# Kernel optimization log

Measured on AMD Instinct MI355X. Metric: run time of the kernel, lower is better.

## Reference

```python
import jax, jax.numpy as jnp
import numpy as np

OUT_CHN, IN_CHN, K = 256, 256, 3
STRIDE, PAD = 1, 1


def setup_inputs() -> dict:
    key = jax.random.key(0)
    kx, kw, ks = jax.random.split(key, 3)
    x = jax.random.normal(kx, (32, IN_CHN, 56, 56), dtype=jnp.float32)
    # flat (out*in*k*k, 1) parameter, small positive init as in the torch module
    weights = jax.random.uniform(kw, (OUT_CHN * IN_CHN * K * K, 1), dtype=jnp.float32) * 0.001
    # real_scaling_factor: mean of a small random (1,out,k,k) tensor over dims 3,2,0 -> (1,out,1,1)
    sf = jax.random.uniform(ks, (1, OUT_CHN, K, K), dtype=jnp.float32) * 0.001
    real_scaling_factor = jnp.mean(jnp.abs(sf), axis=(0, 2, 3), keepdims=True)
    return {"x": x, "weights": weights, "real_scaling_factor": real_scaling_factor}


def reference(x, weights, real_scaling_factor):
    real_w = weights.reshape(OUT_CHN, IN_CHN, K, K)
    # STE binarization: forward value = sign(w), gradient of clamp(w,-1,1)
    clipped = jnp.clip(real_w, -1.0, 1.0)
    binary_w = jax.lax.stop_gradient(jnp.sign(real_w) - clipped) + clipped
    y = jax.lax.conv_general_dilated(
        x, binary_w,
        window_strides=(STRIDE, STRIDE),
        padding=[(PAD, PAD), (PAD, PAD)],
        dimension_numbers=("NCHW", "OIHW", "NCHW"),
    )
    # per-output-channel scale, broadcast over N,H,W
    return y * real_scaling_factor
```

## Files before the change

### kernel.cpp

```cpp
#include <hip/hip_runtime.h>
#include <hip/hip_bf16.h>
#include <stdint.h>

#define NIMG 32
#define CHN 256
#define HW 56
#define PH 58
#define XP_ELEMS ((size_t)NIMG*PH*PH*CHN)
#define WT_ELEMS ((size_t)9*CHN*CHN)
#define OUT_ELEMS ((size_t)NIMG*CHN*HW*HW)
#define NKT 36

typedef __attribute__((ext_vector_type(8))) short short8;
typedef __attribute__((ext_vector_type(4))) float floatx4;

#define GLDS(gp, lbyte) __builtin_amdgcn_global_load_lds( \
    (const __attribute__((address_space(1))) void*)(gp), \
    (__attribute__((address_space(3))) void*)((char*)L + (lbyte)), 16, 0, 0)

__device__ inline unsigned short f2bf(float f) {
    union { float f; uint32_t u; } v; v.f = f;
    uint32_t u = v.u;
    return (unsigned short)((u + 0x7FFFu + ((u >> 16) & 1u)) >> 16);
}

__global__ void wprep(const float* __restrict__ wflat, unsigned short* __restrict__ Wt) {
    int o = blockIdx.x * 256 + threadIdx.x;
    int rs = o >> 16, ko = (o >> 8) & 255, c = o & 255;
    float w = wflat[ko * 2304 + c * 9 + rs];
    Wt[o] = (w > 0.f) ? 0x3F80u : (w < 0.f ? 0xBF80u : 0u);
}

__global__ void halo_zero(unsigned short* __restrict__ Xp) {
    int idx = blockIdx.x * 256 + threadIdx.x;
    int c2 = idx & 127;
    int t  = idx >> 7;
    int ci = t % 228, n = t / 228;
    int h, w;
    if (ci < 58)       { h = 0;        w = ci; }
    else if (ci < 116) { h = 57;       w = ci - 58; }
    else if (ci < 172) { h = ci - 115; w = 0; }
    else               { h = ci - 171; w = 57; }
    *(uint32_t*)&Xp[(((size_t)n * PH + h) * PH + w) * CHN + c2 * 2] = 0u;
}

__global__ void xprep(const float* __restrict__ x, unsigned short* __restrict__ Xp) {
    __shared__ unsigned short tile[56 * 264];
    int b = blockIdx.x;
    int n = b / 56, h = b - n * 56;
    const float* xr = x + ((size_t)n * CHN) * (HW*HW) + h * HW;
    int tid = threadIdx.x;
    #pragma unroll 4
    for (int it = 0; it < 28; ++it) {
        int i = it * 256 + tid;
        int c2 = i / 56, w = i - c2 * 56, c = c2 * 2;
        float f0 = xr[(size_t)c * 3136 + w];
        float f1 = xr[(size_t)(c + 1) * 3136 + w];
        uint32_t u = (uint32_t)f2bf(f0) | ((uint32_t)f2bf(f1) << 16);
        *(uint32_t*)&tile[w * 264 + c] = u;
    }
    __syncthreads();
    unsigned short* op = Xp + (((size_t)n * PH + (h + 1)) * PH + 1) * CHN;
    #pragma unroll
    for (int it = 0; it < 7; ++it) {
        int chunk = it * 256 + tid;
        int w = chunk >> 5, c0 = (chunk & 31) * 8;
        short8 v = *(const short8*)&tile[w * 264 + c0];
        *(short8*)&op[w * 256 + c0] = v;
    }
}

__global__ void __launch_bounds__(512)
bconv8(const unsigned short* __restrict__ Xp, const unsigned short* __restrict__ Wt,
       const float* __restrict__ sf, float* __restrict__ out) {
    extern __shared__ unsigned short L[];
    const int tid  = threadIdx.x;
    const int lane = tid & 63, wv = tid >> 6;
    const int wm = wv >> 2, wn = wv & 3;
    const int bm = blockIdx.x;

    const int r0 = tid >> 3;
    const int sx = (tid & 7) ^ (r0 & 7);
    uint32_t offA[2][2], offB[2][2];
    #pragma unroll
    for (int hf = 0; hf < 2; ++hf)
        #pragma unroll
        for (int i = 0; i < 2; ++i) {
            int row = hf * 128 + i * 64 + r0;
            int p = bm * 256 + row;
            int n = p / 3136, hwp = p - n * 3136;
            int h = hwp / 56,  w = hwp - h * 56;
            offA[hf][i] = (uint32_t)(((((n * 58 + h) * 58 + w) * 256) + sx * 8) * 2);
            offB[hf][i] = (uint32_t)((row * 256 + sx * 8) * 2);
        }
    const uint32_t ldst0 = (uint32_t)wv * 1024u;

#define STAGE_A(kt, hf, b) do { \
    int _rs = (kt) >> 2; int _dr = _rs / 3, _dc = _rs - _dr * 3; \
    uint32_t _ko = (uint32_t)((_dr * 58 + _dc) * 512 + ((kt) & 3) * 128); \
    uint32_t _lb = (uint32_t)(((b) * 4 + (hf)) * 16384) + ldst0; \
    GLDS((const char*)Xp + offA[hf][0] + _ko, _lb); \
    GLDS((const char*)Xp + offA[hf][1] + _ko, _lb + 8192u); \
} while (0)

#define STAGE_B(kt, hf, b) do { \
    uint32_t _ko = (uint32_t)((kt) >> 2) * 131072u + (uint32_t)(((kt) & 3) * 128); \
    uint32_t _lb = (uint32_t)(((b) * 4 + 2 + (hf)) * 16384) + ldst0; \
    GLDS((const char*)Wt + offB[hf][0] + _ko, _lb); \
    GLDS((const char*)Wt + offB[hf][1] + _ko, _lb + 8192u); \
} while (0)

    const int rA = lane & 15, hs = lane >> 4, xm = lane & 7;
    const int sl0 = ((hs)     ^ xm) * 8;
    const int sl1 = ((4 + hs) ^ xm) * 8;

    floatx4 acc[8][4];
    #pragma unroll
    for (int mf = 0; mf < 8; ++mf)
        #pragma unroll
        for (int nf = 0; nf < 4; ++nf) acc[mf][nf] = (floatx4){0.f, 0.f, 0.f, 0.f};

    STAGE_A(0, 0, 0); STAGE_A(0, 1, 0); STAGE_B(0, 0, 0); STAGE_B(0, 1, 0);
    STAGE_A(1, 0, 1); STAGE_A(1, 1, 1); STAGE_B(1, 0, 1); STAGE_B(1, 1, 1);
    asm volatile("s_waitcnt vmcnt(8)" ::: "memory");
    __builtin_amdgcn_s_barrier();

    short8 a0[4][2], a1[4][2], b0[2][2], b1[2][2];

    for (int j = 0; j < NKT; ++j) {
        const int buf = j & 1;
        const uint32_t sA = (uint32_t)(buf * 4 + wm) * 8192u + (uint32_t)(rA * 64);
        const uint32_t sB = (uint32_t)(buf * 4 + 2 + (wn >> 1)) * 8192u
                          + (uint32_t)((wn & 1) * 4096) + (uint32_t)(rA * 64);
        #pragma unroll
        for (int mf = 0; mf < 4; ++mf) {
            a0[mf][0] = *(const short8*)&L[sA + mf * 1024 + sl0];
            a0[mf][1] = *(const short8*)&L[sA + mf * 1024 + sl1];
        }
        #pragma unroll
        for (int nf = 0; nf < 2; ++nf) {
            b0[nf][0] = *(const short8*)&L[sB + nf * 1024 + sl0];
            b0[nf][1] = *(const short8*)&L[sB + nf * 1024 + sl1];
            b1[nf][0] = *(const short8*)&L[sB + (2 + nf) * 1024 + sl0];
            b1[nf][1] = *(const short8*)&L[sB + (2 + nf) * 1024 + sl1];
        }
        asm volatile("s_waitcnt lgkmcnt(0)" ::: "memory");
        __builtin_amdgcn_s_barrier();
        __builtin_amdgcn_s_setprio(1);
        #pragma unroll
        for (int mf = 0; mf < 4; ++mf)
            #pragma unroll
            for (int nf = 0; nf < 2; ++nf) {
                acc[mf][nf] = __builtin_amdgcn_mfma_f32_16x16x32_bf16(a0[mf][0], b0[nf][0], acc[mf][nf], 0, 0, 0);
                acc[mf][nf] = __builtin_amdgcn_mfma_f32_16x16x32_bf16(a0[mf][1], b0[nf][1], acc[mf][nf], 0, 0, 0);
            }
        __builtin_amdgcn_s_setprio(0);
        __builtin_amdgcn_s_barrier();
        #pragma unroll
        for (int mf = 0; mf < 4; ++mf) {
            a1[mf][0] = *(const short8*)&L[sA + (4 + mf) * 1024 + sl0];
            a1[mf][1] = *(const short8*)&L[sA + (4 + mf) * 1024 + sl1];
        }
        if (j < NKT - 2) STAGE_B(j + 2, 0, buf);
        __builtin_amdgcn_s_barrier();
        __builtin_amdgcn_s_setprio(1);
        #pragma unroll
        for (int mf = 0; mf < 4; ++mf)
            #pragma unroll
            for (int nf = 0; nf < 2; ++nf) {
                acc[4 + mf][nf] = __builtin_amdgcn_mfma_f32_16x16x32_bf16(a1[mf][0], b0[nf][0], acc[4 + mf][nf], 0, 0, 0);
                acc[4 + mf][nf] = __builtin_amdgcn_mfma_f32_16x16x32_bf16(a1[mf][1], b0[nf][1], acc[4 + mf][nf], 0, 0, 0);
            }
        __builtin_amdgcn_s_setprio(0);
        __builtin_amdgcn_s_barrier();
        if (j < NKT - 2) { STAGE_B(j + 2, 1, buf); STAGE_A(j + 2, 0, buf); }
        __builtin_amdgcn_s_barrier();
        __builtin_amdgcn_s_setprio(1);
        #pragma unroll
        for (int mf = 0; mf < 4; ++mf)
            #pragma unroll
            for (int nf = 0; nf < 2; ++nf) {
                acc[mf][2 + nf] = __builtin_amdgcn_mfma_f32_16x16x32_bf16(a0[mf][0], b1[nf][0], acc[mf][2 + nf], 0, 0, 0);
                acc[mf][2 + nf] = __builtin_amdgcn_mfma_f32_16x16x32_bf16(a0[mf][1], b1[nf][1], acc[mf][2 + nf], 0, 0, 0);
            }
        __builtin_amdgcn_s_setprio(0);
        __builtin_amdgcn_s_barrier();
        if (j < NKT - 2) {
            STAGE_A(j + 2, 1, buf);
            asm volatile("s_waitcnt vmcnt(8)" ::: "memory");
        } else {
            asm volatile("s_waitcnt vmcnt(0)" ::: "memory");
        }
        __builtin_amdgcn_s_barrier();
        __builtin_amdgcn_s_setprio(1);
        #pragma unroll
        for (int mf = 0; mf < 4; ++mf)
            #pragma unroll
            for (int nf = 0; nf < 2; ++nf) {
                acc[4 + mf][2 + nf] = __builtin_amdgcn_mfma_f32_16x16x32_bf16(a1[mf][0], b1[nf][0], acc[4 + mf][2 + nf], 0, 0, 0);
                acc[4 + mf][2 + nf] = __builtin_amdgcn_mfma_f32_16x16x32_bf16(a1[mf][1], b1[nf][1], acc[4 + mf][2 + nf], 0, 0, 0);
            }
        __builtin_amdgcn_s_setprio(0);
        __builtin_amdgcn_s_barrier();
    }

    const int p00 = bm * 256 + wm * 128 + hs * 4;
    #pragma unroll
    for (int nf = 0; nf < 4; ++nf) {
        int ko = wn * 64 + nf * 16 + rA;
        float sc = sf[ko];
        #pragma unroll
        for (int mf = 0; mf < 8; ++mf) {
            int p = p00 + mf * 16;
            int ni = p / 3136, hwp = p - ni * 3136;
            floatx4 v = acc[mf][nf];
            floatx4 o = {v.x * sc, v.y * sc, v.z * sc, v.w * sc};
            *(floatx4*)&out[(size_t)ni * 802816 + (size_t)ko * 3136 + hwp] = o;
        }
    }
#undef STAGE_A
#undef STAGE_B
}

__global__ void naive_conv(const float* __restrict__ x, const float* __restrict__ wflat,
                           const float* __restrict__ sf, float* __restrict__ out) {
    int idx = blockIdx.x * 256 + threadIdx.x;
    int w = idx % 56, t = idx / 56;
    int h = t % 56; t /= 56;
    int ko = t % 256; int n = t / 256;
    float acc = 0.f;
    for (int c = 0; c < 256; ++c) {
        const float* xc = x + ((size_t)n * 256 + c) * 3136;
        const float* wc = wflat + ((size_t)ko * 256 + c) * 9;
        #pragma unroll
        for (int r = 0; r < 3; ++r) {
            int hh = h + r - 1;
            if (hh < 0 || hh >= 56) continue;
            #pragma unroll
            for (int s = 0; s < 3; ++s) {
                int ww = w + s - 1;
                if (ww < 0 || ww >= 56) continue;
                float wvv = wc[r * 3 + s];
                float sgn = (wvv > 0.f) ? 1.f : ((wvv < 0.f) ? -1.f : 0.f);
                acc += sgn * xc[hh * 56 + ww];
            }
        }
    }
    out[idx] = acc * sf[ko];
}

extern "C" void kernel_launch(void* const* d_in, const int* in_sizes, int n_in,
                              void* d_out, int out_size, void* d_ws, size_t ws_size,
                              hipStream_t stream) {
    const float* x     = (const float*)d_in[0];
    const float* wflat = (const float*)d_in[1];
    const float* sf    = (const float*)d_in[2];
    float* out = (float*)d_out;

    const size_t need = XP_ELEMS * 2 + WT_ELEMS * 2;
    if (ws_size < need) {
        naive_conv<<<(int)(OUT_ELEMS / 256), 256, 0, stream>>>(x, wflat, sf, out);
        return;
    }
    unsigned short* Xp = (unsigned short*)d_ws;
    unsigned short* Wt = Xp + XP_ELEMS;

    (void)hipFuncSetAttribute((const void*)bconv8,
                              hipFuncAttributeMaxDynamicSharedMemorySize, 131072);

    halo_zero<<<(32 * 228 * 128) / 256, 256, 0, stream>>>(Xp);
    wprep<<<2304, 256, 0, stream>>>(wflat, Wt);
    xprep<<<NIMG * HW, 256, 0, stream>>>(x, Xp);
    bconv8<<<392, 512, 131072, stream>>>(Xp, Wt, sf, out);
}
```

Baseline: 339.2 us.

## Halve K-tile to 32 and simplify to single-stage double-buffered pipeline

The K-step shrinks from 64 to 32 channels, giving 72 iterations in place of 36. LDS use is halved to 64KB, which could allow two blocks per CU. The four-phase interleaved staging, with prefetch distance 2 and vmcnt(8), is replaced by a simpler double buffer: prefetch the next tile, run two MFMA halves, then wait for vmcnt(0) and barrier each iteration. This removes several barriers per step, but the wait-for-all every iteration exposes global load latency and doubles the loop overhead per unit of work.

```diff
diff --git a/kernel.cpp b/kernel.cpp
--- a/kernel.cpp
+++ b/kernel.cpp
@@ -9,7 +9,7 @@
 #define XP_ELEMS ((size_t)NIMG*PH*PH*CHN)
 #define WT_ELEMS ((size_t)9*CHN*CHN)
 #define OUT_ELEMS ((size_t)NIMG*CHN*HW*HW)
-#define NKT 36
+#define NKT 72
 
 typedef __attribute__((ext_vector_type(8))) short short8;
 typedef __attribute__((ext_vector_type(4))) float floatx4;
@@ -79,40 +79,36 @@
     const int wm = wv >> 2, wn = wv & 3;
     const int bm = blockIdx.x;
 
-    const int r0 = tid >> 3;
-    const int sx = (tid & 7) ^ (r0 & 7);
-    uint32_t offA[2][2], offB[2][2];
-    #pragma unroll
-    for (int hf = 0; hf < 2; ++hf)
-        #pragma unroll
-        for (int i = 0; i < 2; ++i) {
-            int row = hf * 128 + i * 64 + r0;
-            int p = bm * 256 + row;
-            int n = p / 3136, hwp = p - n * 3136;
-            int h = hwp / 56,  w = hwp - h * 56;
-            offA[hf][i] = (uint32_t)(((((n * 58 + h) * 58 + w) * 256) + sx * 8) * 2);
-            offB[hf][i] = (uint32_t)((row * 256 + sx * 8) * 2);
-        }
+    const int r0 = tid >> 2;
+    const int sx = (tid & 3) ^ (r0 & 3);
+    uint32_t offA[2], offB[2];
+    #pragma unroll
+    for (int i = 0; i < 2; ++i) {
+        int row = i * 128 + r0;
+        int p = bm * 256 + row;
+        int n = p / 3136, hwp = p - n * 3136;
+        int h = hwp / 56,  w = hwp - h * 56;
+        offA[i] = (uint32_t)(((((n * 58 + h) * 58 + w) * 256) + sx * 8) * 2);
+        offB[i] = (uint32_t)((row * 256 + sx * 8) * 2);
+    }
     const uint32_t ldst0 = (uint32_t)wv * 1024u;
 
-#define STAGE_A(kt, hf, b) do { \
-    int _rs = (kt) >> 2; int _dr = _rs / 3, _dc = _rs - _dr * 3; \
-    uint32_t _ko = (uint32_t)((_dr * 58 + _dc) * 512 + ((kt) & 3) * 128); \
-    uint32_t _lb = (uint32_t)(((b) * 4 + (hf)) * 16384) + ldst0; \
-    GLDS((const char*)Xp + offA[hf][0] + _ko, _lb); \
-    GLDS((const char*)Xp + offA[hf][1] + _ko, _lb + 8192u); \
+#define KOA(kt) ({ int _rs = (kt) >> 3; int _dr = _rs / 3, _dc = _rs - _dr * 3; \
+                   (uint32_t)((_dr * 58 + _dc) * 512 + ((kt) & 7) * 64); })
+#define KOB(kt) ((uint32_t)(((kt) >> 3) * 131072 + ((kt) & 7) * 64))
+
+#define STAGE_A(kt, b) do { uint32_t _k = KOA(kt); \
+    GLDS((const char*)Xp + offA[0] + _k, (uint32_t)(b) * 32768u + ldst0); \
+    GLDS((const char*)Xp + offA[1] + _k, (uint32_t)(b) * 32768u + 8192u + ldst0); \
 } while (0)
 
-#define STAGE_B(kt, hf, b) do { \
-    uint32_t _ko = (uint32_t)((kt) >> 2) * 131072u + (uint32_t)(((kt) & 3) * 128); \
-    uint32_t _lb = (uint32_t)(((b) * 4 + 2 + (hf)) * 16384) + ldst0; \
-    GLDS((const char*)Wt + offB[hf][0] + _ko, _lb); \
-    GLDS((const char*)Wt + offB[hf][1] + _ko, _lb + 8192u); \
+#define STAGE_B(kt, b) do { uint32_t _k = KOB(kt); \
+    GLDS((const char*)Wt + offB[0] + _k, (uint32_t)(b) * 32768u + 16384u + ldst0); \
+    GLDS((const char*)Wt + offB[1] + _k, (uint32_t)(b) * 32768u + 24576u + ldst0); \
 } while (0)
 
-    const int rA = lane & 15, hs = lane >> 4, xm = lane & 7;
-    const int sl0 = ((hs)     ^ xm) * 8;
-    const int sl1 = ((4 + hs) ^ xm) * 8;
+    const int rA = lane & 15, hs = lane >> 4;
+    const int slX = (hs ^ (rA & 3)) * 8;
 
     floatx4 acc[8][4];
     #pragma unroll
@@ -120,87 +116,40 @@
         #pragma unroll
         for (int nf = 0; nf < 4; ++nf) acc[mf][nf] = (floatx4){0.f, 0.f, 0.f, 0.f};
 
-    STAGE_A(0, 0, 0); STAGE_A(0, 1, 0); STAGE_B(0, 0, 0); STAGE_B(0, 1, 0);
-    STAGE_A(1, 0, 1); STAGE_A(1, 1, 1); STAGE_B(1, 0, 1); STAGE_B(1, 1, 1);
-    asm volatile("s_waitcnt vmcnt(8)" ::: "memory");
+    STAGE_A(0, 0); STAGE_B(0, 0);
+    asm volatile("s_waitcnt vmcnt(0)" ::: "memory");
     __builtin_amdgcn_s_barrier();
 
-    short8 a0[4][2], a1[4][2], b0[2][2], b1[2][2];
+    short8 a0[4], a1[4], bfr[4];
 
     for (int j = 0; j < NKT; ++j) {
-        const int buf = j & 1;
-        const uint32_t sA = (uint32_t)(buf * 4 + wm) * 8192u + (uint32_t)(rA * 64);
-        const uint32_t sB = (uint32_t)(buf * 4 + 2 + (wn >> 1)) * 8192u
-                          + (uint32_t)((wn & 1) * 4096) + (uint32_t)(rA * 64);
-        #pragma unroll
-        for (int mf = 0; mf < 4; ++mf) {
-            a0[mf][0] = *(const short8*)&L[sA + mf * 1024 + sl0];
-            a0[mf][1] = *(const short8*)&L[sA + mf * 1024 + sl1];
-        }
-        #pragma unroll
-        for (int nf = 0; nf < 2; ++nf) {
-            b0[nf][0] = *(const short8*)&L[sB + nf * 1024 + sl0];
-            b0[nf][1] = *(const short8*)&L[sB + nf * 1024 + sl1];
-            b1[nf][0] = *(const short8*)&L[sB + (2 + nf) * 1024 + sl0];
-            b1[nf][1] = *(const short8*)&L[sB + (2 + nf) * 1024 + sl1];
-        }
-        asm volatile("s_waitcnt lgkmcnt(0)" ::: "memory");
+        const int buf = j & 1, nb = buf ^ 1;
+        const uint32_t sAe = (uint32_t)(buf * 16384) + (uint32_t)((wm * 128 + rA) * 32) + slX;
+        const uint32_t sBe = (uint32_t)(buf * 16384 + 8192) + (uint32_t)((wn * 64 + rA) * 32) + slX;
+        #pragma unroll
+        for (int mf = 0; mf < 4; ++mf) a0[mf] = *(const short8*)&L[sAe + mf * 512];
+        #pragma unroll
+        for (int nf = 0; nf < 4; ++nf) bfr[nf] = *(const short8*)&L[sBe + nf * 512];
+        if (j < NKT - 1) { STAGE_A(j + 1, nb); STAGE_B(j + 1, nb); }
         __builtin_amdgcn_s_barrier();
         __builtin_amdgcn_s_setprio(1);
         #pragma unroll
         for (int mf = 0; mf < 4; ++mf)
             #pragma unroll
-            for (int nf = 0; nf < 2; ++nf) {
-                acc[mf][nf] = __builtin_amdgcn_mfma_f32_16x16x32_bf16(a0[mf][0], b0[nf][0], acc[mf][nf], 0, 0, 0);
-                acc[mf][nf] = __builtin_amdgcn_mfma_f32_16x16x32_bf16(a0[mf][1], b0[nf][1], acc[mf][nf], 0, 0, 0);
-            }
+            for (int nf = 0; nf < 4; ++nf)
+                acc[mf][nf] = __builtin_amdgcn_mfma_f32_16x16x32_bf16(a0[mf], bfr[nf], acc[mf][nf], 0, 0, 0);
         __builtin_amdgcn_s_setprio(0);
         __builtin_amdgcn_s_barrier();
         #pragma unroll
-        for (int mf = 0; mf < 4; ++mf) {
-            a1[mf][0] = *(const short8*)&L[sA + (4 + mf) * 1024 + sl0];
-            a1[mf][1] = *(const short8*)&L[sA + (4 + mf) * 1024 + sl1];
-        }
-        if (j < NKT - 2) STAGE_B(j + 2, 0, buf);
-        __builtin_amdgcn_s_barrier();
+        for (int mf = 0; mf < 4; ++mf) a1[mf] = *(const short8*)&L[sAe + (4 + mf) * 512];
         __builtin_amdgcn_s_setprio(1);
         #pragma unroll
         for (int mf = 0; mf < 4; ++mf)
             #pragma unroll
-            for (int nf = 0; nf < 2; ++nf) {
-                acc[4 + mf][nf] = __builtin_amdgcn_mfma_f32_16x16x32_bf16(a1[mf][0], b0[nf][0], acc[4 + mf][nf], 0, 0, 0);
-                acc[4 + mf][nf] = __builtin_amdgcn_mfma_f32_16x16x32_bf16(a1[mf][1], b0[nf][1], acc[4 + mf][nf], 0, 0, 0);
-            }
+            for (int nf = 0; nf < 4; ++nf)
+                acc[4 + mf][nf] = __builtin_amdgcn_mfma_f32_16x16x32_bf16(a1[mf], bfr[nf], acc[4 + mf][nf], 0, 0, 0);
         __builtin_amdgcn_s_setprio(0);
-        __builtin_amdgcn_s_barrier();
-        if (j < NKT - 2) { STAGE_B(j + 2, 1, buf); STAGE_A(j + 2, 0, buf); }
-        __builtin_amdgcn_s_barrier();
-        __builtin_amdgcn_s_setprio(1);
-        #pragma unroll
-        for (int mf = 0; mf < 4; ++mf)
-            #pragma unroll
-            for (int nf = 0; nf < 2; ++nf) {
-                acc[mf][2 + nf] = __builtin_amdgcn_mfma_f32_16x16x32_bf16(a0[mf][0], b1[nf][0], acc[mf][2 + nf], 0, 0, 0);
-                acc[mf][2 + nf] = __builtin_amdgcn_mfma_f32_16x16x32_bf16(a0[mf][1], b1[nf][1], acc[mf][2 + nf], 0, 0, 0);
-            }
-        __builtin_amdgcn_s_setprio(0);
-        __builtin_amdgcn_s_barrier();
-        if (j < NKT - 2) {
-            STAGE_A(j + 2, 1, buf);
-            asm volatile("s_waitcnt vmcnt(8)" ::: "memory");
-        } else {
-            asm volatile("s_waitcnt vmcnt(0)" ::: "memory");
-        }
-        __builtin_amdgcn_s_barrier();
-        __builtin_amdgcn_s_setprio(1);
-        #pragma unroll
-        for (int mf = 0; mf < 4; ++mf)
-            #pragma unroll
-            for (int nf = 0; nf < 2; ++nf) {
-                acc[4 + mf][2 + nf] = __builtin_amdgcn_mfma_f32_16x16x32_bf16(a1[mf][0], b1[nf][0], acc[4 + mf][2 + nf], 0, 0, 0);
-                acc[4 + mf][2 + nf] = __builtin_amdgcn_mfma_f32_16x16x32_bf16(a1[mf][1], b1[nf][1], acc[4 + mf][2 + nf], 0, 0, 0);
-            }
-        __builtin_amdgcn_s_setprio(0);
+        asm volatile("s_waitcnt vmcnt(0)" ::: "memory");
         __builtin_amdgcn_s_barrier();
     }
 
@@ -220,6 +169,8 @@
     }
 #undef STAGE_A
 #undef STAGE_B
+#undef KOA
+#undef KOB
 }
 
 __global__ void naive_conv(const float* __restrict__ x, const float* __restrict__ wflat,
@@ -266,10 +217,10 @@
     unsigned short* Wt = Xp + XP_ELEMS;
 
     (void)hipFuncSetAttribute((const void*)bconv8,
-                              hipFuncAttributeMaxDynamicSharedMemorySize, 131072);
+                              hipFuncAttributeMaxDynamicSharedMemorySize, 65536);
 
     halo_zero<<<(32 * 228 * 128) / 256, 256, 0, stream>>>(Xp);
     wprep<<<2304, 256, 0, stream>>>(wflat, Wt);
     xprep<<<NIMG * HW, 256, 0, stream>>>(x, Xp);
-    bconv8<<<392, 512, 131072, stream>>>(Xp, Wt, sf, out);
-}
+    bconv8<<<392, 512, 65536, stream>>>(Xp, Wt, sf, out);
+}
```

Result: no change. 336.9 us (-0.7%).
